# Performance work log

Hardware: AMD Instinct MI355X
Metric: run time of the kernel (lower is better)

Reference implementation:

```python
import jax, jax.numpy as jnp
import numpy as np

L = 4          # encoder layers
D = 1280       # d_model
H = 20         # heads
DH = D // H
FF = 5120
MEL = 128
S = 1500       # post-conv seq len
EPS = 1e-6


def quant_per_token(x):
    # dynamic per-token int8 quant: scale = max|x|/127
    s = jnp.max(jnp.abs(x), axis=-1, keepdims=True) / 127.0
    s = jnp.maximum(s, 1e-8)
    q = jnp.clip(jnp.round(x / s), -128, 127)
    return q, s


def w8a8_linear(qx, sx, w, b):
    # per-output-channel int8 weight quant, W8A8 GEMM, fp dequant epilogue
    ws = jnp.maximum(jnp.max(jnp.abs(w), axis=1, keepdims=True) / 127.0, 1e-8)  # [O,1]
    qw = jnp.clip(jnp.round(w / ws), -128, 127)
    y = qx @ qw.T                        # int-valued accum in fp32
    return y * sx * ws[:, 0][None, :] + b[None, :]


def rmsnorm_quant(x, w, b):
    # rms_norm_general: w * x / sqrt(E[x^2]+eps) + b, then per-token quant
    inv = jax.lax.rsqrt(jnp.mean(x * x, axis=-1, keepdims=True) + EPS)
    return quant_per_token(x * inv * w[None, :] + b[None, :])


def conv1d(x, w, b, stride, pad):
    y = jax.lax.conv_general_dilated(x, w, (stride,), [(pad, pad)],
                                     dimension_numbers=('NCW', 'OIW', 'NCW'))
    return y + b[None, :, None]


def setup_inputs() -> dict:
    key = jax.random.key(0)
    ks = jax.random.split(key, 24)
    n = lambda k, sh, sc=0.02: jax.random.normal(k, sh, jnp.float32) * sc
    return {
        'input_features': jax.random.normal(ks[0], (1, MEL, 2 * S), jnp.float32),
        'conv1_w': n(ks[1], (D, MEL, 3)), 'conv1_b': n(ks[2], (D,)),
        'conv2_w': n(ks[3], (D, D, 3)), 'conv2_b': n(ks[4], (D,)),
        'pos_emb': n(ks[5], (S, D)),
        'ln1_w': jnp.ones((L, D)), 'ln1_b': n(ks[6], (L, D)),
        'qkv_w': n(ks[7], (L, 3 * D, D)), 'qkv_b': n(ks[8], (L, 3 * D)),
        'out_w': n(ks[9], (L, D, D)), 'out_b': n(ks[10], (L, D)),
        'ln2_w': jnp.ones((L, D)), 'ln2_b': n(ks[11], (L, D)),
        'fc1_w': n(ks[12], (L, FF, D)), 'fc1_b': n(ks[13], (L, FF)),
        'fc2_w': n(ks[14], (L, D, FF)), 'fc2_b': n(ks[15], (L, D)),
        'lnf_w': jnp.ones((D,)), 'lnf_b': n(ks[16], (D,)),
    }


def reference(input_features, conv1_w, conv1_b, conv2_w, conv2_b, pos_emb,
              ln1_w, ln1_b, qkv_w, qkv_b, out_w, out_b,
              ln2_w, ln2_b, fc1_w, fc1_b, fc2_w, fc2_b, lnf_w, lnf_b):
    B = input_features.shape[0]
    h = jax.nn.gelu(conv1d(input_features, conv1_w, conv1_b, 1, 1))
    h = jax.nn.gelu(conv1d(h, conv2_w, conv2_b, 2, 1))
    h = h.transpose(0, 2, 1) + pos_emb[None]          # [B,S,D]
    h = h.reshape(B * S, D)
    scale = DH ** -0.5
    for l in range(L):
        res = h
        qx, sx = rmsnorm_quant(h, ln1_w[l], ln1_b[l])
        qkv = w8a8_linear(qx, sx, qkv_w[l], qkv_b[l])  # [B*S, 3D]
        q, k, v = jnp.split(qkv.reshape(B, S, 3, H, DH), 3, axis=2)
        q, k, v = q[:, :, 0], k[:, :, 0], v[:, :, 0]   # [B,S,H,DH]
        scores = jnp.einsum('bqhd,bkhd->bhqk', q, k) * scale
        attn = jax.nn.softmax(scores, axis=-1)
        ao = jnp.einsum('bhqk,bkhd->bqhd', attn, v).reshape(B * S, D)
        qa, sa = quant_per_token(ao)
        h = res + w8a8_linear(qa, sa, out_w[l], out_b[l])
        res = h
        qx, sx = rmsnorm_quant(h, ln2_w[l], ln2_b[l])
        f1 = w8a8_linear(qx, sx, fc1_w[l], fc1_b[l])
        qm, sm = quant_per_token(jax.nn.gelu(f1))
        h = res + w8a8_linear(qm, sm, fc2_w[l], fc2_b[l])
    h = h.reshape(B, S, D)
    # avg_pooler: AvgPool1d(kernel=2, stride=2) over time
    h = h.reshape(B, S // 2, 2, D).mean(axis=2)
    # final LayerNorm (true layernorm, fp path)
    mu = jnp.mean(h, axis=-1, keepdims=True)
    var = jnp.mean(jnp.square(h - mu), axis=-1, keepdims=True)
    h = (h - mu) * jax.lax.rsqrt(var + 1e-5) * lnf_w + lnf_b
    return h
```

## Files before the change

### kernel.cpp

```cpp
#include <hip/hip_runtime.h>
#include <stdint.h>

#define S_LEN 1500
#define D_MODEL 1280
#define N_HEAD 20
#define D_HEAD 64
#define FF_DIM 5120
#define N_LAYER 4

typedef int v4i __attribute__((ext_vector_type(4)));
typedef short v8s __attribute__((ext_vector_type(8)));
typedef short v4s __attribute__((ext_vector_type(4)));
typedef float v4f __attribute__((ext_vector_type(4)));
typedef unsigned short ushort_t;


__device__ inline float gelu_tanh(float x) {
    float x3 = x * x * x;
    return 0.5f * x * (1.0f + tanhf(0.7978845608028654f * (x + 0.044715f * x3)));
}

__device__ inline float wred_sum(float v) {
    for (int o = 32; o > 0; o >>= 1) v += __shfl_down(v, o, 64);
    return v;
}
__device__ inline float wred_max(float v) {
    for (int o = 32; o > 0; o >>= 1) v = fmaxf(v, __shfl_down(v, o, 64));
    return v;
}
__device__ inline float block_sum(float v, float* sm4) {
    v = wred_sum(v);
    int w = threadIdx.x >> 6;
    if ((threadIdx.x & 63) == 0) sm4[w] = v;
    __syncthreads();
    float r = sm4[0] + sm4[1] + sm4[2] + sm4[3];
    __syncthreads();
    return r;
}
__device__ inline float block_max(float v, float* sm4) {
    v = wred_max(v);
    int w = threadIdx.x >> 6;
    if ((threadIdx.x & 63) == 0) sm4[w] = v;
    __syncthreads();
    float r = fmaxf(fmaxf(sm4[0], sm4[1]), fmaxf(sm4[2], sm4[3]));
    __syncthreads();
    return r;
}

__device__ inline unsigned short f2bf(float x) {
    unsigned int u = __float_as_uint(x);
    u += 0x7fffu + ((u >> 16) & 1u);
    return (unsigned short)(u >> 16);
}
__device__ inline float bf2f(unsigned short h) {
    return __uint_as_float(((unsigned int)h) << 16);
}

__device__ inline void gload_lds16(const void* g, void* l) {
    __builtin_amdgcn_global_load_lds(
        (const __attribute__((address_space(1))) char*)g,
        (__attribute__((address_space(3))) char*)l, 16, 0, 0);
}


__global__ __launch_bounds__(256) void im2col1_kernel(
    const float* __restrict__ x, unsigned short* __restrict__ Ah,
    unsigned short* __restrict__ Al)
{
    int t = blockIdx.x * 256 + threadIdx.x;
    int col = blockIdx.y;
    if (t >= 3000) return;
    int tap = col >> 7, i = col & 127;
    int src = t - 1 + tap;
    float v = (src >= 0 && src < 3000) ? x[(size_t)i * 3000 + src] : 0.0f;
    unsigned short h = f2bf(v);
    Ah[(size_t)t * 384 + col] = h;
    Al[(size_t)t * 384 + col] = f2bf(v - bf2f(h));
}

__global__ __launch_bounds__(256) void im2col2_kernel(
    const float* __restrict__ g1, unsigned short* __restrict__ Ah,
    unsigned short* __restrict__ Al)
{
    int col = blockIdx.x * 256 + threadIdx.x;
    int t = blockIdx.y;
    if (col >= 3840) return;
    int tap = col / 1280, o = col - tap * 1280;
    int src = 2 * t - 1 + tap;
    float v = (src >= 0 && src < 3000) ? g1[(size_t)src * 1280 + o] : 0.0f;
    unsigned short h = f2bf(v);
    Ah[(size_t)t * 3840 + col] = h;
    Al[(size_t)t * 3840 + col] = f2bf(v - bf2f(h));
}

__global__ __launch_bounds__(256) void wreorder_kernel(
    const float* __restrict__ w, unsigned short* __restrict__ woh,
    unsigned short* __restrict__ wol, int C)
{
    int o = blockIdx.x;
    int KC = 3 * C;
    const float* wr = w + (size_t)o * KC;
    for (int col = threadIdx.x; col < KC; col += 256) {
        int tap = col / C, i = col - tap * C;
        float v = wr[i * 3 + tap];
        unsigned short h = f2bf(v);
        woh[(size_t)o * KC + col] = h;
        wol[(size_t)o * KC + col] = f2bf(v - bf2f(h));
    }
}

template <int EPI>
__global__ __launch_bounds__(256, 2) void gemm_conv_bf16x3(
    const unsigned short* __restrict__ Ah, const unsigned short* __restrict__ Al,
    const unsigned short* __restrict__ Wh, const unsigned short* __restrict__ Wl,
    const float* __restrict__ bias, const float* __restrict__ pos,
    float* __restrict__ out, int M, int N, int K, int nTilesN)
{
    __shared__ unsigned short lds[2][4][128][32];
    int tid = threadIdx.x;
    int lane = tid & 63;
    int wv = tid >> 6;
    int l15 = lane & 15, quad = lane >> 4;
    int wm = wv >> 1, wn = wv & 1;

    int nwg = gridDim.x;
    int cpx = nwg >> 3;
    int bid = blockIdx.x;
    int swz = (bid & 7) * cpx + (bid >> 3);
    int bx = swz % nTilesN, by = swz / nTilesN;
    int m0 = by * 128, n0 = bx * 128;

    const unsigned short* splane = (wv == 0) ? Ah : (wv == 1) ? Al : (wv == 2) ? Wh : Wl;
    int rbase = (wv < 2) ? m0 : n0;
    int rlim  = (wv < 2) ? M : N;
    const unsigned short* srcp[8];
    #pragma unroll
    for (int c = 0; c < 8; c++) {
        int row = rbase + c * 16 + (lane >> 2);
        if (row >= rlim) row = rlim - 1;
        srcp[c] = splane + (size_t)row * K + (lane & 3) * 8;
    }

    auto stage = [&](int nb, int k0) {
        char* lbase = (char*)&lds[nb][wv][0][0];
        #pragma unroll
        for (int c = 0; c < 8; c++)
            gload_lds16(srcp[c] + k0, lbase + c * 1024);
    };

    v4f acc[4][4];
    #pragma unroll
    for (int i = 0; i < 4; i++)
        #pragma unroll
        for (int j = 0; j < 4; j++) acc[i][j] = (v4f){0.0f, 0.0f, 0.0f, 0.0f};

    int nsteps = K >> 5;
    stage(0, 0);
    __syncthreads();
    int cur = 0;
    for (int t = 0; t < nsteps; t++) {
        if (t + 1 < nsteps) stage(cur ^ 1, (t + 1) * 32);
        v8s ah[4], al2[4], bh[4], bl[4];
        #pragma unroll
        for (int i = 0; i < 4; i++) {
            ah[i]  = *(const v8s*)&lds[cur][0][wm * 64 + i * 16 + l15][quad * 8];
            al2[i] = *(const v8s*)&lds[cur][1][wm * 64 + i * 16 + l15][quad * 8];
            bh[i]  = *(const v8s*)&lds[cur][2][wn * 64 + i * 16 + l15][quad * 8];
            bl[i]  = *(const v8s*)&lds[cur][3][wn * 64 + i * 16 + l15][quad * 8];
        }
        #pragma unroll
        for (int i = 0; i < 4; i++)
            #pragma unroll
            for (int j = 0; j < 4; j++) {
                acc[i][j] = __builtin_amdgcn_mfma_f32_16x16x32_bf16(ah[i],  bh[j], acc[i][j], 0, 0, 0);
                acc[i][j] = __builtin_amdgcn_mfma_f32_16x16x32_bf16(al2[i], bh[j], acc[i][j], 0, 0, 0);
                acc[i][j] = __builtin_amdgcn_mfma_f32_16x16x32_bf16(ah[i],  bl[j], acc[i][j], 0, 0, 0);
            }
        __syncthreads();
        cur ^= 1;
    }

    #pragma unroll
    for (int i = 0; i < 4; i++) {
        #pragma unroll
        for (int j = 0; j < 4; j++) {
            int n = n0 + wn * 64 + j * 16 + l15;
            float bn = bias[n];
            #pragma unroll
            for (int r = 0; r < 4; r++) {
                int m = m0 + wm * 64 + i * 16 + quad * 4 + r;
                if (m < M) {
                    float v = gelu_tanh(acc[i][j][r] + bn);
                    if (EPI == 1) v += pos[(size_t)m * N + n];
                    out[(size_t)m * N + n] = v;
                }
            }
        }
    }
}


__global__ __launch_bounds__(256) void wquant_kernel(
    const float* __restrict__ w, int8_t* __restrict__ qw,
    float* __restrict__ ws, int K)
{
    int r = blockIdx.x;
    int tid = threadIdx.x;
    __shared__ float sm4[4];
    const float4* wr = (const float4*)(w + (size_t)r * K);
    int n4 = K >> 2;
    float mx = 0.0f;
    for (int i = tid; i < n4; i += 256) {
        float4 v = wr[i];
        mx = fmaxf(mx, fmaxf(fmaxf(fabsf(v.x), fabsf(v.y)), fmaxf(fabsf(v.z), fabsf(v.w))));
    }
    mx = block_max(mx, sm4);
    float sc = fmaxf(mx / 127.0f, 1e-8f);
    if (tid == 0) ws[r] = sc;
    float rs = 1.0f / sc;
    char4* qr = (char4*)(qw + (size_t)r * K);
    for (int i = tid; i < n4; i += 256) {
        float4 v = wr[i];
        char4 q;
        q.x = (int8_t)fminf(fmaxf(rintf(v.x * rs), -128.0f), 127.0f);
        q.y = (int8_t)fminf(fmaxf(rintf(v.y * rs), -128.0f), 127.0f);
        q.z = (int8_t)fminf(fmaxf(rintf(v.z * rs), -128.0f), 127.0f);
        q.w = (int8_t)fminf(fmaxf(rintf(v.w * rs), -128.0f), 127.0f);
        qr[i] = q;
    }
}

__global__ __launch_bounds__(256) void rmsnorm_quant_kernel(
    const float* __restrict__ x, const float* __restrict__ w,
    const float* __restrict__ b, int8_t* __restrict__ q,
    float* __restrict__ sx)
{
    int s = blockIdx.x;
    int tid = threadIdx.x;
    __shared__ float sm4[4];
    const float* xr = x + (size_t)s * D_MODEL;
    float v[5];
    float ss = 0.0f;
    for (int i = 0; i < 5; i++) {
        float t = xr[tid + 256 * i];
        v[i] = t;
        ss += t * t;
    }
    ss = block_sum(ss, sm4);
    float inv = rsqrtf(ss * (1.0f / 1280.0f) + 1e-6f);
    float mx = 0.0f;
    for (int i = 0; i < 5; i++) {
        int idx = tid + 256 * i;
        float t = v[i] * inv * w[idx] + b[idx];
        v[i] = t;
        mx = fmaxf(mx, fabsf(t));
    }
    mx = block_max(mx, sm4);
    float sc = fmaxf(mx / 127.0f, 1e-8f);
    if (tid == 0) sx[s] = sc;
    float rs = 1.0f / sc;
    for (int i = 0; i < 5; i++) {
        float qv = rintf(v[i] * rs);
        qv = fminf(fmaxf(qv, -128.0f), 127.0f);
        q[(size_t)s * D_MODEL + tid + 256 * i] = (int8_t)qv;
    }
}

template <bool GELU>
__global__ __launch_bounds__(256) void quant_kernel(
    const float* __restrict__ x, int8_t* __restrict__ q,
    float* __restrict__ sx, int Dm)
{
    int s = blockIdx.x;
    int tid = threadIdx.x;
    __shared__ float sm4[4];
    const float4* xr = (const float4*)(x + (size_t)s * Dm);
    int n4 = Dm >> 2;
    float mx = 0.0f;
    for (int i = tid; i < n4; i += 256) {
        float4 t = xr[i];
        if (GELU) { t.x = gelu_tanh(t.x); t.y = gelu_tanh(t.y); t.z = gelu_tanh(t.z); t.w = gelu_tanh(t.w); }
        mx = fmaxf(mx, fmaxf(fmaxf(fabsf(t.x), fabsf(t.y)), fmaxf(fabsf(t.z), fabsf(t.w))));
    }
    mx = block_max(mx, sm4);
    float sc = fmaxf(mx / 127.0f, 1e-8f);
    if (tid == 0) sx[s] = sc;
    float rs = 1.0f / sc;
    char4* qr = (char4*)(q + (size_t)s * Dm);
    for (int i = tid; i < n4; i += 256) {
        float4 t = xr[i];
        if (GELU) { t.x = gelu_tanh(t.x); t.y = gelu_tanh(t.y); t.z = gelu_tanh(t.z); t.w = gelu_tanh(t.w); }
        char4 qq;
        qq.x = (int8_t)fminf(fmaxf(rintf(t.x * rs), -128.0f), 127.0f);
        qq.y = (int8_t)fminf(fmaxf(rintf(t.y * rs), -128.0f), 127.0f);
        qq.z = (int8_t)fminf(fmaxf(rintf(t.z * rs), -128.0f), 127.0f);
        qq.w = (int8_t)fminf(fmaxf(rintf(t.w * rs), -128.0f), 127.0f);
        qr[i] = qq;
    }
}

__global__ __launch_bounds__(256) void gemm_w8a8_mfma(
    const int8_t* __restrict__ qx, const float* __restrict__ sx,
    const int8_t* __restrict__ qw, const float* __restrict__ ws,
    const float* __restrict__ bias, const float* __restrict__ res,
    float* __restrict__ out, int M, int O, int K)
{
    int lane = threadIdx.x & 63;
    int wv = threadIdx.x >> 6;
    int l15 = lane & 15;
    int quad = lane >> 4;
    int m_base = blockIdx.y * 64 + wv * 16;
    int n_base = blockIdx.x * 64;

    int ar = m_base + l15; if (ar >= M) ar = M - 1;
    const int8_t* ap = qx + (size_t)ar * K + quad * 16;
    const int8_t* bp = qw + (size_t)(n_base + l15) * K + quad * 16;
    size_t rowK16 = (size_t)16 * K;

    v4i acc0 = {0, 0, 0, 0}, acc1 = {0, 0, 0, 0}, acc2 = {0, 0, 0, 0}, acc3 = {0, 0, 0, 0};
    int nsteps = K >> 6;
    for (int s = 0; s < nsteps; s++) {
        v4i a  = *(const v4i*)(ap + s * 64);
        v4i b0 = *(const v4i*)(bp + s * 64);
        v4i b1 = *(const v4i*)(bp + rowK16 + s * 64);
        v4i b2 = *(const v4i*)(bp + 2 * rowK16 + s * 64);
        v4i b3 = *(const v4i*)(bp + 3 * rowK16 + s * 64);
        acc0 = __builtin_amdgcn_mfma_i32_16x16x64_i8(a, b0, acc0, 0, 0, 0);
        acc1 = __builtin_amdgcn_mfma_i32_16x16x64_i8(a, b1, acc1, 0, 0, 0);
        acc2 = __builtin_amdgcn_mfma_i32_16x16x64_i8(a, b2, acc2, 0, 0, 0);
        acc3 = __builtin_amdgcn_mfma_i32_16x16x64_i8(a, b3, acc3, 0, 0, 0);
    }

    float sxv[4];
    #pragma unroll
    for (int r = 0; r < 4; r++) {
        int m = m_base + quad * 4 + r;
        sxv[r] = (m < M) ? sx[m] : 0.0f;
    }
    v4i accs[4] = {acc0, acc1, acc2, acc3};
    #pragma unroll
    for (int nb = 0; nb < 4; nb++) {
        int n = n_base + nb * 16 + l15;
        float wn = ws[n];
        float bn = bias[n];
        #pragma unroll
        for (int r = 0; r < 4; r++) {
            int m = m_base + quad * 4 + r;
            if (m < M) {
                float y = (float)accs[nb][r] * sxv[r] * wn + bn;
                if (res) y += res[(size_t)m * O + n];
                out[(size_t)m * O + n] = y;
            }
        }
    }
}

__global__ __launch_bounds__(256, 2) void attn_mfma_kernel(
    const float* __restrict__ qkv, float* __restrict__ ao)
{
    __shared__ ushort_t Kh[64][72], Kl[64][72];
    __shared__ ushort_t Vh[64][72], Vl[64][72];
    __shared__ ushort_t Ph[64][72], Pl[64][72];
    int h = blockIdx.y;
    int q_tile = blockIdx.x;
    int tid = threadIdx.x;
    int lane = tid & 63;
    int wv = tid >> 6;
    int l15 = lane & 15, quad = lane >> 4;

    int qg = q_tile * 64 + wv * 16 + l15;
    int qc = qg < S_LEN ? qg : S_LEN - 1;
    const float* qsrc = qkv + (size_t)qc * 3840 + h * 64;
    v8s qh[2], ql[2];
    #pragma unroll
    for (int ks = 0; ks < 2; ks++) {
        const float4* p4 = (const float4*)(qsrc + ks * 32 + quad * 8);
        float4 a = p4[0], b = p4[1];
        float f[8] = {a.x, a.y, a.z, a.w, b.x, b.y, b.z, b.w};
        #pragma unroll
        for (int j = 0; j < 8; j++) {
            unsigned short hh = f2bf(f[j]);
            qh[ks][j] = (short)hh;
            ql[ks][j] = (short)f2bf(f[j] - bf2f(hh));
        }
    }

    v4f O[4];
    #pragma unroll
    for (int nb = 0; nb < 4; nb++) O[nb] = (v4f){0.0f, 0.0f, 0.0f, 0.0f};
    float m_run[4], l_run[4];
    #pragma unroll
    for (int r = 0; r < 4; r++) { m_run[r] = -INFINITY; l_run[r] = 0.0f; }

    int sk = tid >> 2, sd = (tid & 3) * 16;
    int vk = (tid & 15) * 4, vd = (tid >> 4) * 4;

    for (int kt = 0; kt < 24; kt++) {
        int kbase = kt * 64;
        int krem = S_LEN - kbase;

        __syncthreads();

        {
            int kg2 = kbase + sk;
            int kc2 = kg2 < S_LEN ? kg2 : S_LEN - 1;
            const float* src = qkv + (size_t)kc2 * 3840 + 1280 + h * 64 + sd;
            float f[16];
            *(float4*)&f[0]  = ((const float4*)src)[0];
            *(float4*)&f[4]  = ((const float4*)src)[1];
            *(float4*)&f[8]  = ((const float4*)src)[2];
            *(float4*)&f[12] = ((const float4*)src)[3];
            v8s h0, h1, l0, l1;
            #pragma unroll
            for (int j = 0; j < 8; j++) {
                unsigned short u0 = f2bf(f[j]);
                unsigned short u1 = f2bf(f[8 + j]);
                h0[j] = (short)u0; l0[j] = (short)f2bf(f[j] - bf2f(u0));
                h1[j] = (short)u1; l1[j] = (short)f2bf(f[8 + j] - bf2f(u1));
            }
            *(v8s*)&Kh[sk][sd] = h0; *(v8s*)&Kh[sk][sd + 8] = h1;
            *(v8s*)&Kl[sk][sd] = l0; *(v8s*)&Kl[sk][sd + 8] = l1;
        }
        {
            float vals[4][4];
            #pragma unroll
            for (int i = 0; i < 4; i++) {
                int kg2 = kbase + vk + i;
                int kc2 = kg2 < S_LEN ? kg2 : S_LEN - 1;
                *(float4*)&vals[i][0] =
                    *(const float4*)(qkv + (size_t)kc2 * 3840 + 2560 + h * 64 + vd);
            }
            #pragma unroll
            for (int j = 0; j < 4; j++) {
                v4s hv, lv;
                #pragma unroll
                for (int i = 0; i < 4; i++) {
                    unsigned short u = f2bf(vals[i][j]);
                    hv[i] = (short)u;
                    lv[i] = (short)f2bf(vals[i][j] - bf2f(u));
                }
                *(v4s*)&Vh[vd + j][vk] = hv;
                *(v4s*)&Vl[vd + j][vk] = lv;
            }
        }
        __syncthreads();

        v4f S[4];
        #pragma unroll
        for (int nb = 0; nb < 4; nb++) S[nb] = (v4f){0.0f, 0.0f, 0.0f, 0.0f};
        #pragma unroll
        for (int ks = 0; ks < 2; ks++) {
            #pragma unroll
            for (int nb = 0; nb < 4; nb++) {
                v8s kbh = *(const v8s*)&Kh[nb * 16 + l15][ks * 32 + quad * 8];
                v8s kbl = *(const v8s*)&Kl[nb * 16 + l15][ks * 32 + quad * 8];
                S[nb] = __builtin_amdgcn_mfma_f32_16x16x32_bf16(qh[ks], kbh, S[nb], 0, 0, 0);
                S[nb] = __builtin_amdgcn_mfma_f32_16x16x32_bf16(ql[ks], kbh, S[nb], 0, 0, 0);
                S[nb] = __builtin_amdgcn_mfma_f32_16x16x32_bf16(qh[ks], kbl, S[nb], 0, 0, 0);
            }
        }

        #pragma unroll
        for (int nb = 0; nb < 4; nb++) {
            bool valid = (nb * 16 + l15) < krem;
            #pragma unroll
            for (int r = 0; r < 4; r++) {
                float s = S[nb][r] * 0.125f;
                S[nb][r] = valid ? s : -INFINITY;
            }
        }

        #pragma unroll
        for (int r = 0; r < 4; r++) {
            float t = fmaxf(fmaxf(S[0][r], S[1][r]), fmaxf(S[2][r], S[3][r]));
            #pragma unroll
            for (int msk = 1; msk < 16; msk <<= 1)
                t = fmaxf(t, __shfl_xor(t, msk, 64));
            float mn = fmaxf(m_run[r], t);
            float alpha = __expf(m_run[r] - mn);
            m_run[r] = mn;
            float rs = 0.0f;
            #pragma unroll
            for (int nb = 0; nb < 4; nb++) {
                float p = __expf(S[nb][r] - mn);
                S[nb][r] = p;
                rs += p;
            }
            #pragma unroll
            for (int msk = 1; msk < 16; msk <<= 1)
                rs += __shfl_xor(rs, msk, 64);
            l_run[r] = l_run[r] * alpha + rs;
            #pragma unroll
            for (int nb = 0; nb < 4; nb++) O[nb][r] *= alpha;
        }

        #pragma unroll
        for (int nb = 0; nb < 4; nb++) {
            #pragma unroll
            for (int r = 0; r < 4; r++) {
                float p = S[nb][r];
                unsigned short hp = f2bf(p);
                Ph[wv * 16 + quad * 4 + r][nb * 16 + l15] = hp;
                Pl[wv * 16 + quad * 4 + r][nb * 16 + l15] = f2bf(p - bf2f(hp));
            }
        }
        __syncthreads();

        #pragma unroll
        for (int ks = 0; ks < 2; ks++) {
            v8s pah = *(const v8s*)&Ph[wv * 16 + l15][ks * 32 + quad * 8];
            v8s pal = *(const v8s*)&Pl[wv * 16 + l15][ks * 32 + quad * 8];
            #pragma unroll
            for (int nb = 0; nb < 4; nb++) {
                v8s vbh = *(const v8s*)&Vh[nb * 16 + l15][ks * 32 + quad * 8];
                v8s vbl = *(const v8s*)&Vl[nb * 16 + l15][ks * 32 + quad * 8];
                O[nb] = __builtin_amdgcn_mfma_f32_16x16x32_bf16(pah, vbh, O[nb], 0, 0, 0);
                O[nb] = __builtin_amdgcn_mfma_f32_16x16x32_bf16(pal, vbh, O[nb], 0, 0, 0);
                O[nb] = __builtin_amdgcn_mfma_f32_16x16x32_bf16(pah, vbl, O[nb], 0, 0, 0);
            }
        }
    }

    #pragma unroll
    for (int r = 0; r < 4; r++) {
        int qg2 = q_tile * 64 + wv * 16 + quad * 4 + r;
        if (qg2 < S_LEN) {
            float rl = 1.0f / l_run[r];
            #pragma unroll
            for (int nb = 0; nb < 4; nb++)
                ao[(size_t)qg2 * D_MODEL + h * 64 + nb * 16 + l15] = O[nb][r] * rl;
        }
    }
}

__global__ __launch_bounds__(256) void pool_ln_kernel(
    const float* __restrict__ h, const float* __restrict__ w,
    const float* __restrict__ b, float* __restrict__ out)
{
    int t = blockIdx.x;
    int tid = threadIdx.x;
    __shared__ float sm4[4];
    const float* r0 = h + (size_t)(2 * t) * D_MODEL;
    const float* r1 = r0 + D_MODEL;
    float v[5];
    float s1 = 0.0f;
    for (int i = 0; i < 5; i++) {
        int idx = tid + 256 * i;
        float x = 0.5f * (r0[idx] + r1[idx]);
        v[i] = x;
        s1 += x;
    }
    float mu = block_sum(s1, sm4) * (1.0f / 1280.0f);
    float s2 = 0.0f;
    for (int i = 0; i < 5; i++) {
        float d = v[i] - mu;
        s2 += d * d;
    }
    float var = block_sum(s2, sm4) * (1.0f / 1280.0f);
    float inv = rsqrtf(var + 1e-5f);
    for (int i = 0; i < 5; i++) {
        int idx = tid + 256 * i;
        out[(size_t)t * D_MODEL + idx] = (v[i] - mu) * inv * w[idx] + b[idx];
    }
}


static inline size_t al256(size_t x) { return (x + 255) & ~(size_t)255; }

extern "C" void kernel_launch(void* const* d_in, const int* in_sizes, int n_in,
                              void* d_out, int out_size, void* d_ws, size_t ws_size,
                              hipStream_t stream) {
    const float* in_feat = (const float*)d_in[0];
    const float* conv1_w = (const float*)d_in[1];
    const float* conv1_b = (const float*)d_in[2];
    const float* conv2_w = (const float*)d_in[3];
    const float* conv2_b = (const float*)d_in[4];
    const float* pos_emb = (const float*)d_in[5];
    const float* ln1_w   = (const float*)d_in[6];
    const float* ln1_b   = (const float*)d_in[7];
    const float* qkv_w   = (const float*)d_in[8];
    const float* qkv_b   = (const float*)d_in[9];
    const float* out_w   = (const float*)d_in[10];
    const float* out_b   = (const float*)d_in[11];
    const float* ln2_w   = (const float*)d_in[12];
    const float* ln2_b   = (const float*)d_in[13];
    const float* fc1_w   = (const float*)d_in[14];
    const float* fc1_b   = (const float*)d_in[15];
    const float* fc2_w   = (const float*)d_in[16];
    const float* fc2_b   = (const float*)d_in[17];
    const float* lnf_w   = (const float*)d_in[18];
    const float* lnf_b   = (const float*)d_in[19];
    float* outp = (float*)d_out;

    char* ws = (char*)d_ws;
    size_t off = 0;
    auto carve = [&](size_t bytes) {
        void* p = ws + off;
        off += al256(bytes);
        return p;
    };
    float*  hA      = (float*)carve((size_t)S_LEN * D_MODEL * 4);
    float*  hB      = (float*)carve((size_t)S_LEN * D_MODEL * 4);
    float*  qkvbuf  = (float*)carve((size_t)S_LEN * 3840 * 4);
    float*  aobuf   = (float*)carve((size_t)S_LEN * D_MODEL * 4);
    float*  f1buf   = (float*)carve((size_t)S_LEN * FF_DIM * 4);
    int8_t* q8      = (int8_t*)carve((size_t)S_LEN * FF_DIM);
    float*  sx      = (float*)carve((size_t)S_LEN * 4);
    int8_t* qw_qkv  = (int8_t*)carve((size_t)3840 * 1280);
    float*  ws_qkv  = (float*)carve((size_t)3840 * 4);
    int8_t* qw_out  = (int8_t*)carve((size_t)1280 * 1280);
    float*  ws_out  = (float*)carve((size_t)1280 * 4);
    int8_t* qw_fc1  = (int8_t*)carve((size_t)5120 * 1280);
    float*  ws_fc1  = (float*)carve((size_t)5120 * 4);
    int8_t* qw_fc2  = (int8_t*)carve((size_t)1280 * 5120);
    float*  ws_fc2  = (float*)carve((size_t)1280 * 4);
    (void)ws_size; (void)n_in; (void)in_sizes; (void)out_size;

    unsigned short* A1h = (unsigned short*)q8;
    unsigned short* A1l = A1h + (size_t)3000 * 384;
    unsigned short* W1h = (unsigned short*)aobuf;
    unsigned short* W1l = W1h + (size_t)1280 * 384;
    float* g1 = qkvbuf;
    unsigned short* A2h = (unsigned short*)f1buf;
    unsigned short* A2l = A2h + (size_t)1500 * 3840;
    unsigned short* W2h = (unsigned short*)qkvbuf;
    unsigned short* W2l = W2h + (size_t)1280 * 3840;

    im2col1_kernel<<<dim3(12, 384), 256, 0, stream>>>(in_feat, A1h, A1l);
    wreorder_kernel<<<1280, 256, 0, stream>>>(conv1_w, W1h, W1l, 128);
    gemm_conv_bf16x3<0><<<240, 256, 0, stream>>>(A1h, A1l, W1h, W1l, conv1_b, nullptr, g1, 3000, 1280, 384, 10);
    im2col2_kernel<<<dim3(15, 1500), 256, 0, stream>>>(g1, A2h, A2l);
    wreorder_kernel<<<1280, 256, 0, stream>>>(conv2_w, W2h, W2l, 1280);
    gemm_conv_bf16x3<1><<<120, 256, 0, stream>>>(A2h, A2l, W2h, W2l, conv2_b, pos_emb, hA, 1500, 1280, 3840, 10);

    float* h = hA;
    float* hn = hB;
    const int mtiles = (S_LEN + 63) / 64;

    for (int l = 0; l < N_LAYER; l++) {
        wquant_kernel<<<3840, 256, 0, stream>>>(qkv_w + (size_t)l * 3840 * 1280, qw_qkv, ws_qkv, 1280);
        wquant_kernel<<<1280, 256, 0, stream>>>(out_w + (size_t)l * 1280 * 1280, qw_out, ws_out, 1280);
        wquant_kernel<<<5120, 256, 0, stream>>>(fc1_w + (size_t)l * 5120 * 1280, qw_fc1, ws_fc1, 1280);
        wquant_kernel<<<1280, 256, 0, stream>>>(fc2_w + (size_t)l * 1280 * 5120, qw_fc2, ws_fc2, 5120);

        rmsnorm_quant_kernel<<<S_LEN, 256, 0, stream>>>(h, ln1_w + l * D_MODEL, ln1_b + l * D_MODEL, q8, sx);
        gemm_w8a8_mfma<<<dim3(60, mtiles), 256, 0, stream>>>(q8, sx, qw_qkv, ws_qkv,
            qkv_b + (size_t)l * 3840, nullptr, qkvbuf, S_LEN, 3840, 1280);
        attn_mfma_kernel<<<dim3(24, N_HEAD), 256, 0, stream>>>(qkvbuf, aobuf);
        quant_kernel<false><<<S_LEN, 256, 0, stream>>>(aobuf, q8, sx, D_MODEL);
        gemm_w8a8_mfma<<<dim3(20, mtiles), 256, 0, stream>>>(q8, sx, qw_out, ws_out,
            out_b + (size_t)l * 1280, h, hn, S_LEN, 1280, 1280);
        { float* t = h; h = hn; hn = t; }

        rmsnorm_quant_kernel<<<S_LEN, 256, 0, stream>>>(h, ln2_w + l * D_MODEL, ln2_b + l * D_MODEL, q8, sx);
        gemm_w8a8_mfma<<<dim3(80, mtiles), 256, 0, stream>>>(q8, sx, qw_fc1, ws_fc1,
            fc1_b + (size_t)l * 5120, nullptr, f1buf, S_LEN, 5120, 1280);
        quant_kernel<true><<<S_LEN, 256, 0, stream>>>(f1buf, q8, sx, FF_DIM);
        gemm_w8a8_mfma<<<dim3(20, mtiles), 256, 0, stream>>>(q8, sx, qw_fc2, ws_fc2,
            fc2_b + (size_t)l * 1280, h, hn, S_LEN, 1280, 5120);
        { float* t = h; h = hn; hn = t; }
    }

    pool_ln_kernel<<<750, 256, 0, stream>>>(h, lnf_w, lnf_b, outp);
}
```

Baseline: 2.283 ms.

## Split conv2 bf16x3 GEMM over K into three partials with separate epilogue

The conv2 GEMM (1500x1280x3840) previously launched only 120 workgroups, which cannot fill the GPU. It now splits K into three 1280-wide chunks, launching 360 workgroups that each write fp32 partial sums into scratch buffers reused from hB, aobuf and q8. A new elementwise kernel adds the three partials with the bias, applies GELU and adds the positional embedding. This trades extra partial-sum memory traffic and one more launch for better occupancy on the dominant conv GEMM.

```diff
diff --git a/kernel.cpp b/kernel.cpp
--- a/kernel.cpp
+++ b/kernel.cpp
@@ -109,11 +109,10 @@
     }
 }
 
-template <int EPI>
 __global__ __launch_bounds__(256, 2) void gemm_conv_bf16x3(
     const unsigned short* __restrict__ Ah, const unsigned short* __restrict__ Al,
     const unsigned short* __restrict__ Wh, const unsigned short* __restrict__ Wl,
-    const float* __restrict__ bias, const float* __restrict__ pos,
+    const float* __restrict__ bias,
     float* __restrict__ out, int M, int N, int K, int nTilesN)
 {
     __shared__ unsigned short lds[2][4][128][32];
@@ -190,13 +189,119 @@
             for (int r = 0; r < 4; r++) {
                 int m = m0 + wm * 64 + i * 16 + quad * 4 + r;
                 if (m < M) {
-                    float v = gelu_tanh(acc[i][j][r] + bn);
-                    if (EPI == 1) v += pos[(size_t)m * N + n];
-                    out[(size_t)m * N + n] = v;
+                    out[(size_t)m * N + n] = gelu_tanh(acc[i][j][r] + bn);
                 }
             }
         }
     }
+}
+
+__global__ __launch_bounds__(256, 2) void gemm_conv_splitk(
+    const unsigned short* __restrict__ Ah, const unsigned short* __restrict__ Al,
+    const unsigned short* __restrict__ Wh, const unsigned short* __restrict__ Wl,
+    float* __restrict__ p0, float* __restrict__ p1, float* __restrict__ p2,
+    int M, int N, int Krow, int Kchunk, int nTilesN, int nTilesM)
+{
+    __shared__ unsigned short lds[2][4][128][32];
+    int tid = threadIdx.x;
+    int lane = tid & 63;
+    int wv = tid >> 6;
+    int l15 = lane & 15, quad = lane >> 4;
+    int wm = wv >> 1, wn = wv & 1;
+
+    int nwg = gridDim.x;
+    int cpx = nwg >> 3;
+    int bid = blockIdx.x;
+    int swz = (bid & 7) * cpx + (bid >> 3);
+    int bx = swz % nTilesN;
+    int t2 = swz / nTilesN;
+    int by = t2 % nTilesM;
+    int ks = t2 / nTilesM;
+    int m0 = by * 128, n0 = bx * 128;
+    int kofs = ks * Kchunk;
+
+    const unsigned short* splane = (wv == 0) ? Ah : (wv == 1) ? Al : (wv == 2) ? Wh : Wl;
+    int rbase = (wv < 2) ? m0 : n0;
+    int rlim  = (wv < 2) ? M : N;
+    const unsigned short* srcp[8];
+    #pragma unroll
+    for (int c = 0; c < 8; c++) {
+        int row = rbase + c * 16 + (lane >> 2);
+        if (row >= rlim) row = rlim - 1;
+        srcp[c] = splane + (size_t)row * Krow + (lane & 3) * 8 + kofs;
+    }
+
+    auto stage = [&](int nb, int k0) {
+        char* lbase = (char*)&lds[nb][wv][0][0];
+        #pragma unroll
+        for (int c = 0; c < 8; c++)
+            gload_lds16(srcp[c] + k0, lbase + c * 1024);
+    };
+
+    v4f acc[4][4];
+    #pragma unroll
+    for (int i = 0; i < 4; i++)
+        #pragma unroll
+        for (int j = 0; j < 4; j++) acc[i][j] = (v4f){0.0f, 0.0f, 0.0f, 0.0f};
+
+    int nsteps = Kchunk >> 5;
+    stage(0, 0);
+    __syncthreads();
+    int cur = 0;
+    for (int t = 0; t < nsteps; t++) {
+        if (t + 1 < nsteps) stage(cur ^ 1, (t + 1) * 32);
+        v8s ah[4], al2[4], bh[4], bl[4];
+        #pragma unroll
+        for (int i = 0; i < 4; i++) {
+            ah[i]  = *(const v8s*)&lds[cur][0][wm * 64 + i * 16 + l15][quad * 8];
+            al2[i] = *(const v8s*)&lds[cur][1][wm * 64 + i * 16 + l15][quad * 8];
+            bh[i]  = *(const v8s*)&lds[cur][2][wn * 64 + i * 16 + l15][quad * 8];
+            bl[i]  = *(const v8s*)&lds[cur][3][wn * 64 + i * 16 + l15][quad * 8];
+        }
+        #pragma unroll
+        for (int i = 0; i < 4; i++)
+            #pragma unroll
+            for (int j = 0; j < 4; j++) {
+                acc[i][j] = __builtin_amdgcn_mfma_f32_16x16x32_bf16(ah[i],  bh[j], acc[i][j], 0, 0, 0);
+                acc[i][j] = __builtin_amdgcn_mfma_f32_16x16x32_bf16(al2[i], bh[j], acc[i][j], 0, 0, 0);
+                acc[i][j] = __builtin_amdgcn_mfma_f32_16x16x32_bf16(ah[i],  bl[j], acc[i][j], 0, 0, 0);
+            }
+        __syncthreads();
+        cur ^= 1;
+    }
+
+    float* pp = (ks == 0) ? p0 : (ks == 1) ? p1 : p2;
+    #pragma unroll
+    for (int i = 0; i < 4; i++) {
+        #pragma unroll
+        for (int j = 0; j < 4; j++) {
+            int n = n0 + wn * 64 + j * 16 + l15;
+            #pragma unroll
+            for (int r = 0; r < 4; r++) {
+                int m = m0 + wm * 64 + i * 16 + quad * 4 + r;
+                if (m < M) pp[(size_t)m * N + n] = acc[i][j][r];
+            }
+        }
+    }
+}
+
+__global__ __launch_bounds__(256) void conv2_epi_kernel(
+    const float* __restrict__ p0, const float* __restrict__ p1,
+    const float* __restrict__ p2, const float* __restrict__ bias,
+    const float* __restrict__ pos, float* __restrict__ out)
+{
+    int idx = blockIdx.x * 256 + threadIdx.x;
+    float4 a = ((const float4*)p0)[idx];
+    float4 b = ((const float4*)p1)[idx];
+    float4 c = ((const float4*)p2)[idx];
+    float4 bb = ((const float4*)bias)[idx % 320];
+    float4 pp = ((const float4*)pos)[idx];
+    float4 o;
+    o.x = gelu_tanh(a.x + b.x + c.x + bb.x) + pp.x;
+    o.y = gelu_tanh(a.y + b.y + c.y + bb.y) + pp.y;
+    o.z = gelu_tanh(a.z + b.z + c.z + bb.z) + pp.z;
+    o.w = gelu_tanh(a.w + b.w + c.w + bb.w) + pp.w;
+    ((float4*)out)[idx] = o;
 }
 
 
@@ -625,13 +730,18 @@
     unsigned short* A2l = A2h + (size_t)1500 * 3840;
     unsigned short* W2h = (unsigned short*)qkvbuf;
     unsigned short* W2l = W2h + (size_t)1280 * 3840;
+    float* P2a = hB;
+    float* P2b = aobuf;
+    float* P2c = (float*)q8;
 
     im2col1_kernel<<<dim3(12, 384), 256, 0, stream>>>(in_feat, A1h, A1l);
     wreorder_kernel<<<1280, 256, 0, stream>>>(conv1_w, W1h, W1l, 128);
-    gemm_conv_bf16x3<0><<<240, 256, 0, stream>>>(A1h, A1l, W1h, W1l, conv1_b, nullptr, g1, 3000, 1280, 384, 10);
+    gemm_conv_bf16x3<<<240, 256, 0, stream>>>(A1h, A1l, W1h, W1l, conv1_b, g1, 3000, 1280, 384, 10);
     im2col2_kernel<<<dim3(15, 1500), 256, 0, stream>>>(g1, A2h, A2l);
     wreorder_kernel<<<1280, 256, 0, stream>>>(conv2_w, W2h, W2l, 1280);
-    gemm_conv_bf16x3<1><<<120, 256, 0, stream>>>(A2h, A2l, W2h, W2l, conv2_b, pos_emb, hA, 1500, 1280, 3840, 10);
+    gemm_conv_splitk<<<360, 256, 0, stream>>>(A2h, A2l, W2h, W2l, P2a, P2b, P2c,
+                                              1500, 1280, 3840, 1280, 10, 12);
+    conv2_epi_kernel<<<1875, 256, 0, stream>>>(P2a, P2b, P2c, conv2_b, pos_emb, hA);
 
     float* h = hA;
     float* hn = hB;
```

Measured after the change: 2.200 ms. 1.04x faster.
